# Performance work log

Hardware: AMD Instinct MI355X
Metric: run time of the kernel (lower is better)

## Reference

```python
import jax, jax.numpy as jnp
import numpy as np

N = 50000        # nodes
E = 800000       # edges (before self loops)
F_IN = 128       # input feature dim
HID = 64         # hidden channels per head
HEADS = 4        # heads for layers 1,2 (conv_out has 1 head)
OUT = 40         # num classes
NEG_SLOPE = 0.2  # PyG GATConv default LeakyReLU slope


def gat_layer(x, src, dst, W, att_src, att_dst, b, num_nodes):
    """PyG-style GATConv (concat=True, inference: no dropout).

    x: [N, F_in], W: [F_in, H*C], att_*: [H, C], b: [H*C].
    """
    H, C = att_src.shape
    xw = (x @ W).reshape(num_nodes, H, C)            # [N, H, C]
    a_s = jnp.sum(xw * att_src[None], axis=-1)       # [N, H] per-node src logit
    a_d = jnp.sum(xw * att_dst[None], axis=-1)       # [N, H] per-node dst logit
    e = jax.nn.leaky_relu(a_s[src] + a_d[dst], NEG_SLOPE)  # [E, H]
    # segment softmax over incoming edges of each dst node
    emax = jax.ops.segment_max(e, dst, num_segments=num_nodes)   # [N, H]
    ee = jnp.exp(e - emax[dst])                                  # [E, H]
    denom = jax.ops.segment_sum(ee, dst, num_segments=num_nodes) # [N, H]
    alpha = ee / (denom[dst] + 1e-16)                            # [E, H]
    # scatter-weighted aggregation of source features
    msg = alpha[:, :, None] * xw[src]                            # [E, H, C]
    out = jax.ops.segment_sum(msg, dst, num_segments=num_nodes)  # [N, H, C]
    return out.reshape(num_nodes, H * C) + b


def setup_inputs() -> dict:
    key = jax.random.key(0)
    ks = jax.random.split(key, 12)

    def glorot(k, shape):
        lim = float(np.sqrt(6.0 / (shape[0] + shape[-1])))
        return jax.random.uniform(k, shape, jnp.float32, -lim, lim)

    x = jax.random.normal(ks[0], (N, F_IN), jnp.float32)
    edge_index = jax.random.randint(ks[1], (2, E), 0, N, dtype=jnp.int32)
    inp = {
        "x": x,
        "edge_index": edge_index,
        # layer 1: 128 -> 4 heads x 64
        "W1": glorot(ks[2], (F_IN, HEADS * HID)),
        "a1_src": glorot(ks[3], (HEADS, HID)),
        "a1_dst": glorot(ks[4], (HEADS, HID)),
        "b1": jnp.zeros((HEADS * HID,), jnp.float32),
        # layer 2: 256 -> 4 heads x 64
        "W2": glorot(ks[5], (HEADS * HID, HEADS * HID)),
        "a2_src": glorot(ks[6], (HEADS, HID)),
        "a2_dst": glorot(ks[7], (HEADS, HID)),
        "b2": jnp.zeros((HEADS * HID,), jnp.float32),
        # output layer: 256 -> 1 head x 40
        "W3": glorot(ks[8], (HEADS * HID, OUT)),
        "a3_src": glorot(ks[9], (1, OUT)),
        "a3_dst": glorot(ks[10], (1, OUT)),
        "b3": jnp.zeros((OUT,), jnp.float32),
    }
    return inp


def reference(x, edge_index, W1, a1_src, a1_dst, b1, W2, a2_src, a2_dst, b2,
              W3, a3_src, a3_dst, b3):
    # PyG GATConv adds self loops by default
    loop = jnp.arange(N, dtype=edge_index.dtype)
    src = jnp.concatenate([edge_index[0], loop])
    dst = jnp.concatenate([edge_index[1], loop])

    h = jax.nn.elu(gat_layer(x, src, dst, W1, a1_src, a1_dst, b1, N))
    h = jax.nn.elu(gat_layer(h, src, dst, W2, a2_src, a2_dst, b2, N))
    h = gat_layer(h, src, dst, W3, a3_src, a3_dst, b3, N)
    return jax.nn.log_softmax(h, axis=1)
```

## Files before the change

### kernel.cpp

```cpp
#include <hip/hip_runtime.h>
#include <hip/hip_bf16.h>

#define NN 50000
#define NE 800000

using bf16x8 = __attribute__((ext_vector_type(8))) short;
using f32x4  = __attribute__((ext_vector_type(4))) float;

__device__ __forceinline__ ushort f2bf(float f) {
  uint x = __float_as_uint(f);
  return (ushort)((x + 0x7FFFu + ((x >> 16) & 1u)) >> 16);
}
__device__ __forceinline__ float bf2f(ushort u) {
  return __uint_as_float(((uint)u) << 16);
}
__device__ __forceinline__ float leaky(float x) { return fmaxf(x, 0.2f * x); }

__device__ __forceinline__ void gload_lds16(const void* g, void* l) {
  __builtin_amdgcn_global_load_lds(
      (const __attribute__((address_space(1))) unsigned int*)g,
      (__attribute__((address_space(3))) unsigned int*)l, 16, 0, 0);
}


__global__ __launch_bounds__(256) void hist_kernel(const int* __restrict__ dst,
                                                   int* __restrict__ counts) {
  int e = blockIdx.x * 256 + threadIdx.x;
  if (e < NE) atomicAdd(&counts[dst[e]], 1);
}

__global__ __launch_bounds__(1024) void scan1_kernel(const int* __restrict__ counts,
                                                     int* __restrict__ partial,
                                                     int* __restrict__ blockSums) {
  __shared__ int sm[1024];
  int i = blockIdx.x * 1024 + threadIdx.x;
  sm[threadIdx.x] = (i < NN) ? counts[i] : 0;
  __syncthreads();
  for (int off = 1; off < 1024; off <<= 1) {
    int t = (threadIdx.x >= off) ? sm[threadIdx.x - off] : 0;
    __syncthreads();
    sm[threadIdx.x] += t;
    __syncthreads();
  }
  if (i < NN) partial[i] = sm[threadIdx.x];
  if (threadIdx.x == 1023) blockSums[blockIdx.x] = sm[1023];
}

__global__ __launch_bounds__(256) void scan23_kernel(const int* __restrict__ partial,
                                                     const int* __restrict__ blockSums,
                                                     int* __restrict__ rowPtr) {
  int i = blockIdx.x * 256 + threadIdx.x;
  if (i < NN) {
    const int nb = i >> 10;
    int off = 0;
    for (int b = 0; b < nb; ++b) off += blockSums[b];
    rowPtr[i + 1] = partial[i] + off;
    if (i == 0) rowPtr[0] = 0;
  }
}

__global__ __launch_bounds__(256) void fill_kernel(const int* __restrict__ srcArr,
                                                   const int* __restrict__ dstArr,
                                                   const int* __restrict__ rowPtr,
                                                   int* __restrict__ cursor,
                                                   int* __restrict__ colSrc) {
  int e = blockIdx.x * 256 + threadIdx.x;
  if (e < NE) {
    int d = dstArr[e];
    int p = rowPtr[d] + atomicAdd(&cursor[d], 1);
    colSrc[p] = srcArr[e];
  }
}


__device__ __forceinline__ void prefrag_one(int idx, const float* __restrict__ W,
                                            const float* __restrict__ atS,
                                            const float* __restrict__ atD,
                                            ushort* __restrict__ Bf,
                                            int Mout, int Mpad, int nh, int Cdim, int KC) {
  const int i = idx & 7;
  const int lane = (idx >> 3) & 63;
  const int kc = (idx >> 9) % KC;
  const int ct = idx / (KC * 512);
  const int k = kc * 32 + (lane >> 4) * 8 + i;
  const int col = ct * 16 + (lane & 15);
  float v = 0.f;
  if (col < Mout) {
    v = W[(size_t)k * Mout + col];
  } else if (col >= Mpad && col < Mpad + nh) {
    const int h = col - Mpad; float s = 0.f;
    for (int c = 0; c < Cdim; ++c) s += W[(size_t)k * Mout + h * Cdim + c] * atS[h * Cdim + c];
    v = s;
  } else if (col >= Mpad + nh && col < Mpad + 2 * nh) {
    const int h = col - Mpad - nh; float s = 0.f;
    for (int c = 0; c < Cdim; ++c) s += W[(size_t)k * Mout + h * Cdim + c] * atD[h * Cdim + c];
    v = s;
  }
  Bf[idx] = f2bf(v);
}

#define T1 (17 * 4 * 512)
#define T2 (17 * 8 * 512)
#define T3 (5 * 8 * 512)

__global__ __launch_bounds__(256) void prefrag_all_kernel(
    const float* __restrict__ W1, const float* __restrict__ a1s, const float* __restrict__ a1d,
    const float* __restrict__ W2, const float* __restrict__ a2s, const float* __restrict__ a2d,
    const float* __restrict__ W3, const float* __restrict__ a3s, const float* __restrict__ a3d,
    ushort* __restrict__ Bf1, ushort* __restrict__ Bf2, ushort* __restrict__ Bf3) {
  int idx = blockIdx.x * 256 + threadIdx.x;
  if (idx < T1) {
    prefrag_one(idx, W1, a1s, a1d, Bf1, 256, 256, 4, 64, 4);
  } else if (idx < T1 + T2) {
    prefrag_one(idx - T1, W2, a2s, a2d, Bf2, 256, 256, 4, 64, 8);
  } else if (idx < T1 + T2 + T3) {
    prefrag_one(idx - T1 - T2, W3, a3s, a3d, Bf3, 40, 64, 1, 40, 8);
  }
}


template <int NCT, int KC, bool AF32>
__global__ __launch_bounds__(256) void gemm_mfma_kernel(const void* __restrict__ Araw,
                                                        const ushort* __restrict__ Bf,
                                                        ushort* __restrict__ xw,
                                                        float* __restrict__ asB,
                                                        float* __restrict__ adB,
                                                        int Mpad, int nh) {
  __shared__ __align__(16) ushort sB[2][NCT * 512];
  constexpr int K = KC * 32;
  const int lane = threadIdx.x & 63;
  const int w = threadIdx.x >> 6;
  const int rowBase = blockIdx.x * 64 + w * 16;
  const int arow = min(rowBase + (lane & 15), NN - 1);
  const int koff = (lane >> 4) * 8;
  f32x4 acc[NCT];
#pragma unroll
  for (int ct = 0; ct < NCT; ++ct) acc[ct] = (f32x4){0.f, 0.f, 0.f, 0.f};

#pragma unroll
  for (int ct0 = 0; ct0 < NCT; ++ct0) {
    if ((ct0 & 3) == w)
      gload_lds16(Bf + (((size_t)ct0 * KC) << 9) + lane * 8, &sB[0][ct0 * 512]);
  }
  __syncthreads();

#pragma unroll
  for (int kc = 0; kc < KC; ++kc) {
    const int nb = kc & 1;
    if (kc + 1 < KC) {
#pragma unroll
      for (int ct0 = 0; ct0 < NCT; ++ct0) {
        if ((ct0 & 3) == w)
          gload_lds16(Bf + (((size_t)ct0 * KC + kc + 1) << 9) + lane * 8,
                      &sB[nb ^ 1][ct0 * 512]);
      }
    }
    bf16x8 af;
    if constexpr (AF32) {
      const float* ap = (const float*)Araw + (size_t)arow * K + koff + kc * 32;
      float4 p0 = *(const float4*)ap;
      float4 p1 = *(const float4*)(ap + 4);
      af[0] = (short)f2bf(p0.x); af[1] = (short)f2bf(p0.y);
      af[2] = (short)f2bf(p0.z); af[3] = (short)f2bf(p0.w);
      af[4] = (short)f2bf(p1.x); af[5] = (short)f2bf(p1.y);
      af[6] = (short)f2bf(p1.z); af[7] = (short)f2bf(p1.w);
    } else {
      const ushort* ap = (const ushort*)Araw + (size_t)arow * K + koff + kc * 32;
      af = *reinterpret_cast<const bf16x8*>(ap);
    }
#pragma unroll
    for (int ct = 0; ct < NCT; ++ct) {
      bf16x8 bfr = *reinterpret_cast<const bf16x8*>(&sB[nb][ct * 512 + lane * 8]);
      acc[ct] = __builtin_amdgcn_mfma_f32_16x16x32_bf16(af, bfr, acc[ct], 0, 0, 0);
    }
    __syncthreads();
  }

  const int colL = lane & 15;
  const int rquad = (lane >> 4) * 4;
#pragma unroll
  for (int ct = 0; ct < NCT; ++ct) {
    const int col = ct * 16 + colL;
#pragma unroll
    for (int r = 0; r < 4; ++r) {
      const int row = rowBase + rquad + r;
      if (row < NN) {
        const float v = acc[ct][r];
        if (col < Mpad) {
          xw[(size_t)row * Mpad + col] = f2bf(v);
        } else if (col < Mpad + nh) {
          asB[(size_t)row * nh + (col - Mpad)] = v;
        } else if (col < Mpad + 2 * nh) {
          adB[(size_t)row * nh + (col - Mpad - nh)] = v;
        }
      }
    }
  }
}


__global__ __launch_bounds__(256) void aggregate256_kernel(
    const ushort* __restrict__ xw, const float* __restrict__ asB, const float* __restrict__ adB,
    const int* __restrict__ rowPtr, const int* __restrict__ colSrc,
    const float* __restrict__ bias, ushort* __restrict__ hout, int applyElu) {
  __shared__ int   lsrc[4][64];
  __shared__ float lw[4][256];
  const int n = (blockIdx.x * blockDim.x + threadIdx.x) >> 6;
  if (n >= NN) return;
  const int lane = threadIdx.x & 63;
  const int wv = (threadIdx.x >> 6) & 3;
  const int h = lane >> 4;
  const int ch = lane * 4;
  const int p0 = rowPtr[n], deg = rowPtr[n + 1] - p0;
  const float4 ad4 = *(const float4*)(adB + n * 4);
  const float4 as4 = *(const float4*)(asB + n * 4);
  float4 m;
  m.x = leaky(as4.x + ad4.x); m.y = leaky(as4.y + ad4.y);
  m.z = leaky(as4.z + ad4.z); m.w = leaky(as4.w + ad4.w);
  float4 s = make_float4(1.f, 1.f, 1.f, 1.f);
  ushort4 xv4 = *(const ushort4*)(xw + (size_t)n * 256 + ch);
  float4 acc = make_float4(bf2f(xv4.x), bf2f(xv4.y), bf2f(xv4.z), bf2f(xv4.w));

  for (int c0 = 0; c0 < deg; c0 += 64) {
    const int e = c0 + lane;
    const bool valid = e < deg;
    const int src = valid ? colSrc[p0 + e] : n;
    const float4 a4 = *(const float4*)(asB + src * 4);
    float4 ev;
    ev.x = valid ? leaky(a4.x + ad4.x) : -3.0e38f;
    ev.y = valid ? leaky(a4.y + ad4.y) : -3.0e38f;
    ev.z = valid ? leaky(a4.z + ad4.z) : -3.0e38f;
    ev.w = valid ? leaky(a4.w + ad4.w) : -3.0e38f;
    float4 mc = ev;
#pragma unroll
    for (int o = 1; o < 64; o <<= 1) {
      mc.x = fmaxf(mc.x, __shfl_xor(mc.x, o));
      mc.y = fmaxf(mc.y, __shfl_xor(mc.y, o));
      mc.z = fmaxf(mc.z, __shfl_xor(mc.z, o));
      mc.w = fmaxf(mc.w, __shfl_xor(mc.w, o));
    }
    float4 m2;
    m2.x = fmaxf(m.x, mc.x); m2.y = fmaxf(m.y, mc.y);
    m2.z = fmaxf(m.z, mc.z); m2.w = fmaxf(m.w, mc.w);
    float4 sc;
    sc.x = __expf(m.x - m2.x); sc.y = __expf(m.y - m2.y);
    sc.z = __expf(m.z - m2.z); sc.w = __expf(m.w - m2.w);
    const float msc = (h == 0) ? sc.x : (h == 1) ? sc.y : (h == 2) ? sc.z : sc.w;
    acc.x *= msc; acc.y *= msc; acc.z *= msc; acc.w *= msc;
    float4 w4;
    w4.x = valid ? __expf(ev.x - m2.x) : 0.f;
    w4.y = valid ? __expf(ev.y - m2.y) : 0.f;
    w4.z = valid ? __expf(ev.z - m2.z) : 0.f;
    w4.w = valid ? __expf(ev.w - m2.w) : 0.f;
    lsrc[wv][lane] = src;
    *(float4*)&lw[wv][lane * 4] = make_float4(w4.x, w4.y, w4.z, w4.w);
    float4 ss = w4;
#pragma unroll
    for (int o = 1; o < 64; o <<= 1) {
      ss.x += __shfl_xor(ss.x, o);
      ss.y += __shfl_xor(ss.y, o);
      ss.z += __shfl_xor(ss.z, o);
      ss.w += __shfl_xor(ss.w, o);
    }
    s.x = s.x * sc.x + ss.x; s.y = s.y * sc.y + ss.y;
    s.z = s.z * sc.z + ss.z; s.w = s.w * sc.w + ss.w;
    m = m2;
    const int cd = min(64, deg - c0);
    const int cdr = (cd + 7) & ~7;
    for (int j = 0; j < cdr; j += 8) {
      int ssrc[8]; float wj[8];
#pragma unroll
      for (int q = 0; q < 8; ++q) {
        ssrc[q] = lsrc[wv][j + q];
        wj[q] = lw[wv][(j + q) * 4 + h];
      }
      ushort4 u[8];
#pragma unroll
      for (int q = 0; q < 8; ++q)
        u[q] = *(const ushort4*)(xw + (size_t)ssrc[q] * 256 + ch);
#pragma unroll
      for (int q = 0; q < 8; ++q) {
        acc.x += wj[q] * bf2f(u[q].x);
        acc.y += wj[q] * bf2f(u[q].y);
        acc.z += wj[q] * bf2f(u[q].z);
        acc.w += wj[q] * bf2f(u[q].w);
      }
    }
  }

  const float sh = (h == 0) ? s.x : (h == 1) ? s.y : (h == 2) ? s.z : s.w;
  const float inv = 1.f / (sh + 1e-16f);
  const float4 b4 = *(const float4*)(bias + ch);
  float o0 = acc.x * inv + b4.x, o1 = acc.y * inv + b4.y;
  float o2 = acc.z * inv + b4.z, o3 = acc.w * inv + b4.w;
  if (applyElu) {
    o0 = o0 > 0.f ? o0 : __expf(o0) - 1.f;
    o1 = o1 > 0.f ? o1 : __expf(o1) - 1.f;
    o2 = o2 > 0.f ? o2 : __expf(o2) - 1.f;
    o3 = o3 > 0.f ? o3 : __expf(o3) - 1.f;
  }
  ushort4 o4;
  o4.x = f2bf(o0); o4.y = f2bf(o1); o4.z = f2bf(o2); o4.w = f2bf(o3);
  *(ushort4*)(hout + (size_t)n * 256 + ch) = o4;
}


__global__ __launch_bounds__(256) void aggregate40_lsm_kernel(
    const ushort* __restrict__ xw, const float* __restrict__ asB, const float* __restrict__ adB,
    const int* __restrict__ rowPtr, const int* __restrict__ colSrc,
    const float* __restrict__ bias, float* __restrict__ out) {
  __shared__ int   lsrc[4][64];
  __shared__ float lw[4][64];
  const int n = (blockIdx.x * blockDim.x + threadIdx.x) >> 6;
  if (n >= NN) return;
  const int lane = threadIdx.x & 63;
  const int wv = (threadIdx.x >> 6) & 3;
  const bool act = lane < 40;
  const int p0 = rowPtr[n], deg = rowPtr[n + 1] - p0;
  const float adn = adB[n];
  float m = leaky(asB[n] + adn);
  float s = 1.f;
  float acc = bf2f(xw[(size_t)n * 64 + lane]);

  for (int c0 = 0; c0 < deg; c0 += 64) {
    const int e = c0 + lane;
    const bool valid = e < deg;
    const int src = valid ? colSrc[p0 + e] : n;
    const float a = asB[src];
    float ev = valid ? leaky(a + adn) : -3.0e38f;
    float mc = ev;
#pragma unroll
    for (int o = 1; o < 64; o <<= 1) mc = fmaxf(mc, __shfl_xor(mc, o));
    const float m2 = fmaxf(m, mc);
    const float scl = __expf(m - m2);
    acc *= scl;
    float wv_ = valid ? __expf(ev - m2) : 0.f;
    lsrc[wv][lane] = src;
    lw[wv][lane] = wv_;
    float ss = wv_;
#pragma unroll
    for (int o = 1; o < 64; o <<= 1) ss += __shfl_xor(ss, o);
    s = s * scl + ss;
    m = m2;
    const int cd = min(64, deg - c0);
    const int cdr = (cd + 7) & ~7;
    for (int j = 0; j < cdr; j += 8) {
      int ssrc[8]; float wj[8];
#pragma unroll
      for (int q = 0; q < 8; ++q) { ssrc[q] = lsrc[wv][j + q]; wj[q] = lw[wv][j + q]; }
      ushort u[8];
#pragma unroll
      for (int q = 0; q < 8; ++q) u[q] = xw[(size_t)ssrc[q] * 64 + lane];
#pragma unroll
      for (int q = 0; q < 8; ++q) acc += wj[q] * bf2f(u[q]);
    }
  }

  float val = acc / (s + 1e-16f) + (act ? bias[lane] : 0.f);
  float v = act ? val : -1e30f;
  float mx = v;
#pragma unroll
  for (int o = 1; o < 64; o <<= 1) mx = fmaxf(mx, __shfl_xor(mx, o));
  float ex = act ? __expf(val - mx) : 0.f;
#pragma unroll
  for (int o = 1; o < 64; o <<= 1) ex += __shfl_xor(ex, o);
  if (act) out[(size_t)n * 40 + lane] = val - mx - __logf(ex);
}


extern "C" void kernel_launch(void* const* d_in, const int* in_sizes, int n_in,
                              void* d_out, int out_size, void* d_ws, size_t ws_size,
                              hipStream_t stream) {
  const float* x   = (const float*)d_in[0];
  const int*   ei  = (const int*)d_in[1];
  const float* W1  = (const float*)d_in[2];
  const float* a1s = (const float*)d_in[3];
  const float* a1d = (const float*)d_in[4];
  const float* b1  = (const float*)d_in[5];
  const float* W2  = (const float*)d_in[6];
  const float* a2s = (const float*)d_in[7];
  const float* a2d = (const float*)d_in[8];
  const float* b2  = (const float*)d_in[9];
  const float* W3  = (const float*)d_in[10];
  const float* a3s = (const float*)d_in[11];
  const float* a3d = (const float*)d_in[12];
  const float* b3  = (const float*)d_in[13];
  float* out = (float*)d_out;

  char* w = (char*)d_ws;
  ushort* xwBuf = (ushort*)w;  w += (size_t)NN * 256 * 2;
  ushort* hBuf  = (ushort*)w;  w += (size_t)NN * 256 * 2;
  ushort* xw40  = (ushort*)w;  w += (size_t)NN * 64 * 2;
  float* asBuf  = (float*)w;   w += (size_t)NN * 4 * 4;
  float* adBuf  = (float*)w;   w += (size_t)NN * 4 * 4;
  ushort* Bf1   = (ushort*)w;  w += (size_t)T1 * 2;
  ushort* Bf2   = (ushort*)w;  w += (size_t)T2 * 2;
  ushort* Bf3   = (ushort*)w;  w += (size_t)T3 * 2;
  int* counts   = (int*)w;     w += (size_t)NN * 4;
  int* cursor   = (int*)w;     w += (size_t)NN * 4;
  int* rowPtr   = (int*)w;     w += (size_t)(NN + 1) * 4;
  int* colSrc   = (int*)w;     w += (size_t)NE * 4;
  int* partial  = (int*)w;     w += (size_t)NN * 4;
  int* blockSums = (int*)w;    w += 64 * 4;

  const int nScanBlocks = (NN + 1023) / 1024;

  hipMemsetAsync(counts, 0, (size_t)2 * NN * 4, stream);
  hist_kernel<<<(NE + 255) / 256, 256, 0, stream>>>(ei + NE, counts);
  scan1_kernel<<<nScanBlocks, 1024, 0, stream>>>(counts, partial, blockSums);
  scan23_kernel<<<(NN + 255) / 256, 256, 0, stream>>>(partial, blockSums, rowPtr);
  fill_kernel<<<(NE + 255) / 256, 256, 0, stream>>>(ei, ei + NE, rowPtr, cursor, colSrc);

  prefrag_all_kernel<<<(T1 + T2 + T3 + 255) / 256, 256, 0, stream>>>(
      W1, a1s, a1d, W2, a2s, a2d, W3, a3s, a3d, Bf1, Bf2, Bf3);

  const int gemmBlocks = (NN + 63) / 64;
  const int nodeBlocks = NN / 4;

  gemm_mfma_kernel<17, 4, true><<<gemmBlocks, 256, 0, stream>>>(x, Bf1, xwBuf, asBuf, adBuf, 256, 4);
  aggregate256_kernel<<<nodeBlocks, 256, 0, stream>>>(xwBuf, asBuf, adBuf, rowPtr, colSrc, b1, hBuf, 1);

  gemm_mfma_kernel<17, 8, false><<<gemmBlocks, 256, 0, stream>>>(hBuf, Bf2, xwBuf, asBuf, adBuf, 256, 4);
  aggregate256_kernel<<<nodeBlocks, 256, 0, stream>>>(xwBuf, asBuf, adBuf, rowPtr, colSrc, b2, hBuf, 1);

  gemm_mfma_kernel<5, 8, false><<<gemmBlocks, 256, 0, stream>>>(hBuf, Bf3, xw40, asBuf, adBuf, 64, 1);
  aggregate40_lsm_kernel<<<nodeBlocks, 256, 0, stream>>>(xw40, asBuf, adBuf, rowPtr, colSrc, b3, out);
}
```

Measured before the change: 419.9 us.

## Store layer-1/2 projected features as FP8 and enlarge GEMM blocks to 512 threads

The projected node features for the two 256-wide layers are now written by the GEMM as FP8 (one byte per value) instead of bf16. The aggregation kernels read them back with packed FP8-to-f32 conversions. This halves the bytes of the gather-heavy edge aggregation, which likely dominates runtime. The GEMM blocks also grow to 8 waves covering 128 rows, so each B tile is shared by more rows. FP8 storage reduces feature precision and risks accuracy-tolerance failures.

```diff
diff --git a/kernel.cpp b/kernel.cpp
--- a/kernel.cpp
+++ b/kernel.cpp
@@ -6,6 +6,7 @@
 
 using bf16x8 = __attribute__((ext_vector_type(8))) short;
 using f32x4  = __attribute__((ext_vector_type(4))) float;
+using f32x2  = __attribute__((ext_vector_type(2))) float;
 
 __device__ __forceinline__ ushort f2bf(float f) {
   uint x = __float_as_uint(f);
@@ -15,6 +16,16 @@
   return __uint_as_float(((uint)u) << 16);
 }
 __device__ __forceinline__ float leaky(float x) { return fmaxf(x, 0.2f * x); }
+
+__device__ __forceinline__ unsigned char f32_to_fp8(float v) {
+  int pk = __builtin_amdgcn_cvt_pk_fp8_f32(v, v, 0, false);
+  return (unsigned char)(pk & 0xff);
+}
+__device__ __forceinline__ float4 fp8x4_to_f32(uint u) {
+  f32x2 lo = __builtin_amdgcn_cvt_pk_f32_fp8((int)u, false);
+  f32x2 hi = __builtin_amdgcn_cvt_pk_f32_fp8((int)u, true);
+  return make_float4(lo[0], lo[1], hi[0], hi[1]);
+}
 
 __device__ __forceinline__ void gload_lds16(const void* g, void* l) {
   __builtin_amdgcn_global_load_lds(
@@ -119,10 +130,10 @@
 }
 
 
-template <int NCT, int KC, bool AF32>
-__global__ __launch_bounds__(256) void gemm_mfma_kernel(const void* __restrict__ Araw,
+template <int NCT, int KC, bool AF32, bool OUT8>
+__global__ __launch_bounds__(512) void gemm_mfma_kernel(const void* __restrict__ Araw,
                                                         const ushort* __restrict__ Bf,
-                                                        ushort* __restrict__ xw,
+                                                        void* __restrict__ xwOut,
                                                         float* __restrict__ asB,
                                                         float* __restrict__ adB,
                                                         int Mpad, int nh) {
@@ -130,7 +141,7 @@
   constexpr int K = KC * 32;
   const int lane = threadIdx.x & 63;
   const int w = threadIdx.x >> 6;
-  const int rowBase = blockIdx.x * 64 + w * 16;
+  const int rowBase = blockIdx.x * 128 + w * 16;
   const int arow = min(rowBase + (lane & 15), NN - 1);
   const int koff = (lane >> 4) * 8;
   f32x4 acc[NCT];
@@ -139,7 +150,7 @@
 
 #pragma unroll
   for (int ct0 = 0; ct0 < NCT; ++ct0) {
-    if ((ct0 & 3) == w)
+    if ((ct0 & 7) == w)
       gload_lds16(Bf + (((size_t)ct0 * KC) << 9) + lane * 8, &sB[0][ct0 * 512]);
   }
   __syncthreads();
@@ -150,7 +161,7 @@
     if (kc + 1 < KC) {
 #pragma unroll
       for (int ct0 = 0; ct0 < NCT; ++ct0) {
-        if ((ct0 & 3) == w)
+        if ((ct0 & 7) == w)
           gload_lds16(Bf + (((size_t)ct0 * KC + kc + 1) << 9) + lane * 8,
                       &sB[nb ^ 1][ct0 * 512]);
       }
@@ -187,7 +198,11 @@
       if (row < NN) {
         const float v = acc[ct][r];
         if (col < Mpad) {
-          xw[(size_t)row * Mpad + col] = f2bf(v);
+          if constexpr (OUT8) {
+            ((unsigned char*)xwOut)[(size_t)row * Mpad + col] = f32_to_fp8(v);
+          } else {
+            ((ushort*)xwOut)[(size_t)row * Mpad + col] = f2bf(v);
+          }
         } else if (col < Mpad + nh) {
           asB[(size_t)row * nh + (col - Mpad)] = v;
         } else if (col < Mpad + 2 * nh) {
@@ -200,7 +215,8 @@
 
 
 __global__ __launch_bounds__(256) void aggregate256_kernel(
-    const ushort* __restrict__ xw, const float* __restrict__ asB, const float* __restrict__ adB,
+    const unsigned char* __restrict__ xw, const float* __restrict__ asB,
+    const float* __restrict__ adB,
     const int* __restrict__ rowPtr, const int* __restrict__ colSrc,
     const float* __restrict__ bias, ushort* __restrict__ hout, int applyElu) {
   __shared__ int   lsrc[4][64];
@@ -218,8 +234,7 @@
   m.x = leaky(as4.x + ad4.x); m.y = leaky(as4.y + ad4.y);
   m.z = leaky(as4.z + ad4.z); m.w = leaky(as4.w + ad4.w);
   float4 s = make_float4(1.f, 1.f, 1.f, 1.f);
-  ushort4 xv4 = *(const ushort4*)(xw + (size_t)n * 256 + ch);
-  float4 acc = make_float4(bf2f(xv4.x), bf2f(xv4.y), bf2f(xv4.z), bf2f(xv4.w));
+  float4 acc = fp8x4_to_f32(*(const uint*)(xw + (size_t)n * 256 + ch));
 
   for (int c0 = 0; c0 < deg; c0 += 64) {
     const int e = c0 + lane;
@@ -274,16 +289,17 @@
         ssrc[q] = lsrc[wv][j + q];
         wj[q] = lw[wv][(j + q) * 4 + h];
       }
-      ushort4 u[8];
+      uint u[8];
 #pragma unroll
       for (int q = 0; q < 8; ++q)
-        u[q] = *(const ushort4*)(xw + (size_t)ssrc[q] * 256 + ch);
+        u[q] = *(const uint*)(xw + (size_t)ssrc[q] * 256 + ch);
 #pragma unroll
       for (int q = 0; q < 8; ++q) {
-        acc.x += wj[q] * bf2f(u[q].x);
-        acc.y += wj[q] * bf2f(u[q].y);
-        acc.z += wj[q] * bf2f(u[q].z);
-        acc.w += wj[q] * bf2f(u[q].w);
+        const float4 x4 = fp8x4_to_f32(u[q]);
+        acc.x += wj[q] * x4.x;
+        acc.y += wj[q] * x4.y;
+        acc.z += wj[q] * x4.z;
+        acc.w += wj[q] * x4.w;
       }
     }
   }
@@ -388,7 +404,7 @@
   float* out = (float*)d_out;
 
   char* w = (char*)d_ws;
-  ushort* xwBuf = (ushort*)w;  w += (size_t)NN * 256 * 2;
+  unsigned char* xwBuf = (unsigned char*)w;  w += (size_t)NN * 256;
   ushort* hBuf  = (ushort*)w;  w += (size_t)NN * 256 * 2;
   ushort* xw40  = (ushort*)w;  w += (size_t)NN * 64 * 2;
   float* asBuf  = (float*)w;   w += (size_t)NN * 4 * 4;
@@ -414,15 +430,15 @@
   prefrag_all_kernel<<<(T1 + T2 + T3 + 255) / 256, 256, 0, stream>>>(
       W1, a1s, a1d, W2, a2s, a2d, W3, a3s, a3d, Bf1, Bf2, Bf3);
 
-  const int gemmBlocks = (NN + 63) / 64;
+  const int gemmBlocks = (NN + 127) / 128;
   const int nodeBlocks = NN / 4;
 
-  gemm_mfma_kernel<17, 4, true><<<gemmBlocks, 256, 0, stream>>>(x, Bf1, xwBuf, asBuf, adBuf, 256, 4);
+  gemm_mfma_kernel<17, 4, true, true><<<gemmBlocks, 512, 0, stream>>>(x, Bf1, xwBuf, asBuf, adBuf, 256, 4);
   aggregate256_kernel<<<nodeBlocks, 256, 0, stream>>>(xwBuf, asBuf, adBuf, rowPtr, colSrc, b1, hBuf, 1);
 
-  gemm_mfma_kernel<17, 8, false><<<gemmBlocks, 256, 0, stream>>>(hBuf, Bf2, xwBuf, asBuf, adBuf, 256, 4);
+  gemm_mfma_kernel<17, 8, false, true><<<gemmBlocks, 512, 0, stream>>>(hBuf, Bf2, xwBuf, asBuf, adBuf, 256, 4);
   aggregate256_kernel<<<nodeBlocks, 256, 0, stream>>>(xwBuf, asBuf, adBuf, rowPtr, colSrc, b2, hBuf, 1);
 
-  gemm_mfma_kernel<5, 8, false><<<gemmBlocks, 256, 0, stream>>>(hBuf, Bf3, xw40, asBuf, adBuf, 64, 1);
+  gemm_mfma_kernel<5, 8, false, false><<<gemmBlocks, 512, 0, stream>>>(hBuf, Bf3, xw40, asBuf, adBuf, 64, 1);
   aggregate40_lsm_kernel<<<nodeBlocks, 256, 0, stream>>>(xw40, asBuf, adBuf, rowPtr, colSrc, b3, out);
 }
```

New measurement: 389.3 us. -7.3%, faster.
